# Kernel optimization log

Measured on AMD Instinct MI355X. Metric: run time of the kernel, lower is better.

Reference implementation:

```python
import jax, jax.numpy as jnp
import numpy as np

HASH_CODE_LEN = 8  # config['hash_code_len']
EPS = 1e-12

def _l2norm(x):
    n = jnp.sqrt(jnp.sum(x * x, axis=-1, keepdims=True))
    return x / jnp.maximum(n, EPS)

def setup_inputs() -> dict:
    key = jax.random.key(0)
    k1, k2, k3, k4 = jax.random.split(key, 4)
    B, H, S, D = 2, 12, 2048, 64
    Q = jax.random.normal(k1, (B, H, S, D), dtype=jnp.float32)
    K = jax.random.normal(k2, (B, H, S, D), dtype=jnp.float32)
    V = jax.random.normal(k3, (B, H, S, D), dtype=jnp.float32)
    mask = jnp.ones((B, S), dtype=jnp.float32)
    conv_w = jax.random.normal(k4, (H, 1, 3, 1), dtype=jnp.float32)  # depthwise Conv2d weight [H,1,w,1]
    return {"Q": Q, "K": K, "V": V, "mask": mask, "conv_w": conv_w}

def reference(Q, K, V, mask, conv_w):
    B, H, S, D = Q.shape
    # conv branch: depthwise conv over the sequence axis, per head (groups=num_head)
    Vm = V * mask[:, None, :, None]  # [B,H,S,D]
    conv_V = jax.lax.conv_general_dilated(
        Vm, conv_w,
        window_strides=(1, 1),
        padding=[(1, 1), (0, 0)],  # (conv_window//2, 0)
        dimension_numbers=("NCHW", "OIHW", "NCHW"),
        feature_group_count=H,
    )
    # YOSO attention: exact expectation of LSH cumulation.
    # collision prob of unit vectors q,k over hash_code_len bits: (1 - acos(q.k)/pi)^tau
    qn = _l2norm(Q)
    kn = _l2norm(K)
    dots = jnp.einsum("bhsd,bhtd->bhst", qn, kn)
    dots = jnp.clip(dots, -1.0, 1.0)
    W = (1.0 - jnp.arccos(dots) / jnp.pi) ** HASH_CODE_LEN  # [B,H,S,S]
    W = W * mask[:, None, None, :]  # key mask
    X = jnp.einsum("bhst,bhtd->bhsd", W, V)
    X = X * mask[:, None, :, None]  # query mask
    X = _l2norm(X)  # kernel.normalize(X)
    return X + conv_V
```

## Files before the change

### kernel.cpp

```cpp
#include <hip/hip_runtime.h>
#include <hip/hip_bf16.h>
#include <math.h>

#define NB 2
#define NH 12
#define NS 2048
#define ND 64
#define NBH (NB * NH)
#define TILE_USHORT 4096
#define QK_TILE_BLOCKS 1536
#define V_BLOCKS (NBH * 32)

typedef __attribute__((ext_vector_type(8))) short short8;
typedef __attribute__((ext_vector_type(4))) float floatx4;
typedef __attribute__((ext_vector_type(2))) float float2v;

__device__ __forceinline__ unsigned short f32_to_bf16_rne(float f) {
  unsigned int u = __float_as_uint(f);
  u += 0x7fffu + ((u >> 16) & 1u);
  return (unsigned short)(u >> 16);
}

__device__ __forceinline__ unsigned int bf16rne_bits(float f) {
  unsigned int u = __float_as_uint(f);
  return u + 0x7fffu + ((u >> 16) & 1u);
}

__device__ __forceinline__ unsigned int pack2_bf16_rne(float lo, float hi) {
  return __builtin_amdgcn_perm(bf16rne_bits(hi), bf16rne_bits(lo), 0x07060302);
}

__device__ __forceinline__ unsigned int pack_bf16_trunc(float lo, float hi) {
  return __builtin_amdgcn_perm(__float_as_uint(hi), __float_as_uint(lo), 0x07060302);
}

__device__ __forceinline__ float2v mk2(float x) { return (float2v){x, x}; }
__device__ __forceinline__ float2v max2(float2v a, float2v b) {
  return (float2v){fmaxf(a[0], b[0]), fmaxf(a[1], b[1])};
}
__device__ __forceinline__ float2v abs2(float2v a) {
  return (float2v){fabsf(a[0]), fabsf(a[1])};
}

__device__ __forceinline__ float yoso_f_exact(float d) {
  const float c0 = 0.49996030f;
  const float c1 = -0.06751822f;
  const float c2 = 0.02363774f;
  const float c3 = -0.00596174f;
  float a = fminf(fabsf(d), 1.0f);
  float p = fmaf(fmaf(fmaf(c3, a, c2), a, c1), a, c0);
  float u = sqrtf(1.0f - a) * p;
  return (d >= 0.0f) ? (1.0f - u) : u;
}

__device__ __forceinline__ void gload_lds16(const unsigned short* src,
                                            unsigned short* lds_dst) {
  __builtin_amdgcn_global_load_lds(
      (const __attribute__((address_space(1))) unsigned int*)(const void*)src,
      (__attribute__((address_space(3))) unsigned int*)(void*)lds_dst,
      16, 0, 0);
}

__global__ __launch_bounds__(256) void prep_all(
    const float* __restrict__ Q, const float* __restrict__ K,
    const float* __restrict__ V, const float* __restrict__ mask,
    unsigned short* __restrict__ qimg, unsigned short* __restrict__ kimg,
    unsigned short* __restrict__ vimg) {
  int blk = blockIdx.x;
  if (blk < QK_TILE_BLOCKS) {
    const float* src = Q;
    unsigned short* dst = qimg;
    if (blk >= 768) { src = K; dst = kimg; blk -= 768; }
    int ti  = blk;
    int tid = threadIdx.x;
    int w   = tid >> 6;
    int l   = tid & 63;
    int nl  = l & 15;
    int dq  = l >> 4;

    const float* row = src + ((size_t)ti * 64 + w * 16 + nl) * ND + dq * 8;
    float4 a0 = *(const float4*)(row);
    float4 a1 = *(const float4*)(row + 4);
    float4 b0 = *(const float4*)(row + 32);
    float4 b1 = *(const float4*)(row + 36);

    float ss = a0.x*a0.x + a0.y*a0.y + a0.z*a0.z + a0.w*a0.w
             + a1.x*a1.x + a1.y*a1.y + a1.z*a1.z + a1.w*a1.w
             + b0.x*b0.x + b0.y*b0.y + b0.z*b0.z + b0.w*b0.w
             + b1.x*b1.x + b1.y*b1.y + b1.z*b1.z + b1.w*b1.w;
    ss += __shfl_xor(ss, 16, 64);
    ss += __shfl_xor(ss, 32, 64);
    float rn = 1.0f / fmaxf(sqrtf(ss), 1e-12f);

    uint4 o0, o1;
    o0.x = pack2_bf16_rne(a0.x * rn, a0.y * rn);
    o0.y = pack2_bf16_rne(a0.z * rn, a0.w * rn);
    o0.z = pack2_bf16_rne(a1.x * rn, a1.y * rn);
    o0.w = pack2_bf16_rne(a1.z * rn, a1.w * rn);
    o1.x = pack2_bf16_rne(b0.x * rn, b0.y * rn);
    o1.y = pack2_bf16_rne(b0.z * rn, b0.w * rn);
    o1.z = pack2_bf16_rne(b1.x * rn, b1.y * rn);
    o1.w = pack2_bf16_rne(b1.z * rn, b1.w * rn);

    unsigned short* op = dst + (size_t)ti * TILE_USHORT + w * 512 + l * 8;
    *(uint4*)(op)            = o0;
    *(uint4*)(op + 4 * 512)  = o1;
  } else {
    int vb = blk - QK_TILE_BLOCKS;
    int bh = vb >> 5, kt = vb & 31, t0 = kt * 64;
    int b  = bh / NH;
    __shared__ float sT[64][65];
    int tid = threadIdx.x;
    int tr = tid >> 2;
    int dc = (tid & 3) * 16;
    float m = mask[b * NS + t0 + tr];
    const float* vp = V + ((size_t)bh * NS + t0 + tr) * ND + dc;
    #pragma unroll
    for (int jj = 0; jj < 16; jj += 4) {
      float4 v = *(const float4*)(vp + jj);
      sT[dc + jj + 0][tr] = v.x * m;
      sT[dc + jj + 1][tr] = v.y * m;
      sT[dc + jj + 2][tr] = v.z * m;
      sT[dc + jj + 3][tr] = v.w * m;
    }
    __syncthreads();
    int dr = tid >> 2;
    unsigned short* op = vimg + (size_t)(bh * 32 + kt) * TILE_USHORT;
    #pragma unroll
    for (int g = 0; g < 2; ++g) {
      int combo = (tid & 3) * 2 + g;
      int kk2 = combo >> 2;
      int qd  = combo & 3;
      uint4 u;
      int tb = kk2 * 32 + qd * 4;
      u.x = (unsigned int)f32_to_bf16_rne(sT[dr][tb + 0]) |
            ((unsigned int)f32_to_bf16_rne(sT[dr][tb + 1]) << 16);
      u.y = (unsigned int)f32_to_bf16_rne(sT[dr][tb + 2]) |
            ((unsigned int)f32_to_bf16_rne(sT[dr][tb + 3]) << 16);
      u.z = (unsigned int)f32_to_bf16_rne(sT[dr][tb + 16]) |
            ((unsigned int)f32_to_bf16_rne(sT[dr][tb + 17]) << 16);
      u.w = (unsigned int)f32_to_bf16_rne(sT[dr][tb + 18]) |
            ((unsigned int)f32_to_bf16_rne(sT[dr][tb + 19]) << 16);
      int frag = kk2 * 4 + (dr >> 4);
      int ln   = qd * 16 + (dr & 15);
      *(uint4*)(op + frag * 512 + ln * 8) = u;
    }
  }
}

__global__ __launch_bounds__(512, 6) void yoso_main(
    const unsigned short* __restrict__ qimg, const unsigned short* __restrict__ kimg,
    const unsigned short* __restrict__ vimg, const float* __restrict__ V,
    const float* __restrict__ mask, const float* __restrict__ conv_w,
    float* __restrict__ out) {
  int bid = blockIdx.x;
  int lid = (bid & 7) * 96 + (bid >> 3);
  int bh = lid >> 5;
  int b  = bh / NH;
  int h  = bh % NH;
  int qt = lid & 31;
  int s0 = qt * 64;

  __shared__ unsigned short kstage[2][4096];

  int tid  = threadIdx.x;
  int wv   = tid >> 6;
  int lane = tid & 63;
  int lq   = lane & 15;
  int quad = lane >> 4;
  int j    = wv & 3;
  int tk   = wv >> 2;

  uint4 qfrag[2];
  {
    const unsigned short* qtile = qimg + (size_t)(bh * 32 + qt) * TILE_USHORT;
    #pragma unroll
    for (int kk = 0; kk < 2; ++kk)
      qfrag[kk] = *(const uint4*)(qtile + (kk * 4 + j) * 512 + lane * 8);
  }

  float w0 = conv_w[h * 3 + 0], w1 = conv_w[h * 3 + 1], w2 = conv_w[h * 3 + 2];

  floatx4 acc[4];
  #pragma unroll
  for (int fd = 0; fd < 4; ++fd) acc[fd] = (floatx4){0.f, 0.f, 0.f, 0.f};

  const unsigned short* kb  = kimg + (size_t)bh * 32 * TILE_USHORT;
  const unsigned short* vbI = vimg + (size_t)bh * 32 * TILE_USHORT;

  const float P0 = 0.3183098862f;
  const float P1 = 0.0530516477f;
  const float P2 = 0.0238732415f;
  const float P3 = 0.0142098402f;
  const float P4 = 0.0096701727f;
  const float P5 = 0.0071212906f;

  auto stage_tile = [&](int buf, int kt) {
    gload_lds16(kb + (size_t)kt * TILE_USHORT + wv * 512 + lane * 8,
                &kstage[buf][wv * 512]);
  };

  stage_tile(0, 0);
  __syncthreads();

  #pragma unroll 1
  for (int kt = 0; kt < 32; ++kt) {
    int cur = kt & 1;
    if (kt < 31) stage_tile(cur ^ 1, kt + 1);

    const unsigned short* sb = kstage[cur];

    uint4 kf[2][2];
    #pragma unroll
    for (int kk = 0; kk < 2; ++kk)
      #pragma unroll
      for (int fl = 0; fl < 2; ++fl)
        kf[kk][fl] = *(const uint4*)(sb + (kk * 4 + tk * 2 + fl) * 512 + lane * 8);

    floatx4 sc[2];
    #pragma unroll
    for (int fl = 0; fl < 2; ++fl) sc[fl] = (floatx4){0.f, 0.f, 0.f, 0.f};
    #pragma unroll
    for (int kk = 0; kk < 2; ++kk) {
      short8 bq = *(const short8*)&qfrag[kk];
      #pragma unroll
      for (int fl = 0; fl < 2; ++fl)
        sc[fl] = __builtin_amdgcn_mfma_f32_16x16x32_bf16(
            *(const short8*)&kf[kk][fl], bq, sc[fl], 0, 0, 0);
    }

    const unsigned short* vtile = vbI + (size_t)kt * TILE_USHORT;
    uint4 vf[4];
    #pragma unroll
    for (int fd = 0; fd < 4; ++fd)
      vf[fd] = *(const uint4*)(vtile + (tk * 4 + fd) * 512 + lane * 8);

    {
      float2v mxy = mk2(0.f);
      #pragma unroll
      for (int fl = 0; fl < 2; ++fl) {
        float2v* p = (float2v*)&sc[fl];
        mxy = max2(mxy, max2(abs2(p[0]), abs2(p[1])));
      }
      float mx = fmaxf(mxy[0], mxy[1]);
      if (__builtin_expect(__any(mx > 0.82f), 0)) {
        #pragma unroll
        for (int fl = 0; fl < 2; ++fl)
          #pragma unroll
          for (int r2 = 0; r2 < 4; ++r2) {
            float f = yoso_f_exact(sc[fl][r2]);
            float f2 = f * f;
            float f4 = f2 * f2;
            sc[fl][r2] = f4 * f4;
          }
      } else {
        float2v c5 = mk2(P5), c4 = mk2(P4), c3 = mk2(P3), c2 = mk2(P2),
                c1 = mk2(P1), c0 = mk2(P0), hf = mk2(0.5f);
        #pragma unroll
        for (int fl = 0; fl < 2; ++fl) {
          float2v* p = (float2v*)&sc[fl];
          #pragma unroll
          for (int hh = 0; hh < 2; ++hh) {
            float2v d = p[hh];
            float2v y = d * d;
            float2v pp = ((((c5 * y + c4) * y + c3) * y + c2) * y + c1) * y + c0;
            float2v f = pp * d + hf;
            float2v f2 = f * f;
            float2v f4 = f2 * f2;
            p[hh] = f4 * f4;
          }
        }
      }
    }

    {
      uint4 u;
      u.x = pack_bf16_trunc(sc[0][0], sc[0][1]);
      u.y = pack_bf16_trunc(sc[0][2], sc[0][3]);
      u.z = pack_bf16_trunc(sc[1][0], sc[1][1]);
      u.w = pack_bf16_trunc(sc[1][2], sc[1][3]);
      short8 bw = *(short8*)&u;
      #pragma unroll
      for (int fd = 0; fd < 4; ++fd)
        acc[fd] = __builtin_amdgcn_mfma_f32_16x16x32_bf16(
            *(const short8*)&vf[fd], bw, acc[fd], 0, 0, 0);
    }

    __syncthreads();
  }

  float* xch = (float*)&kstage[0][0];
  if (tk == 1) {
    float* wr = xch + (j << 10);
    #pragma unroll
    for (int fd = 0; fd < 4; ++fd)
      #pragma unroll
      for (int r2 = 0; r2 < 4; ++r2)
        wr[(fd * 16 + quad * 4 + r2) * 16 + lq] = acc[fd][r2];
  }
  __syncthreads();
  if (tk == 0) {
    const float* rd = xch + (j << 10);
    #pragma unroll
    for (int fd = 0; fd < 4; ++fd)
      #pragma unroll
      for (int r2 = 0; r2 < 4; ++r2)
        acc[fd][r2] += rd[(fd * 16 + quad * 4 + r2) * 16 + lq];

    int s = s0 + j * 16 + lq;
    float qm  = mask[b * NS + s];
    float qm0 = (s > 0) ? mask[b * NS + s - 1] : 0.f;
    float qm2 = (s < NS - 1) ? mask[b * NS + s + 1] : 0.f;
    float ssum = 0.f;
    #pragma unroll
    for (int fd = 0; fd < 4; ++fd)
      #pragma unroll
      for (int r2 = 0; r2 < 4; ++r2) {
        float x = acc[fd][r2] * qm;
        acc[fd][r2] = x;
        ssum += x * x;
      }
    ssum += __shfl_xor(ssum, 16, 64);
    ssum += __shfl_xor(ssum, 32, 64);
    float rn = 1.0f / fmaxf(sqrtf(ssum), 1e-12f);

    const float* vfull = V + ((size_t)bh * NS + s) * ND;
    #pragma unroll
    for (int fd = 0; fd < 4; ++fd) {
      int d = fd * 16 + quad * 4;
      float4 vc1 = *(const float4*)(vfull + d);
      float4 cv;
      cv.x = w1 * vc1.x * qm; cv.y = w1 * vc1.y * qm;
      cv.z = w1 * vc1.z * qm; cv.w = w1 * vc1.w * qm;
      if (s > 0) {
        float4 vc0 = *(const float4*)(vfull - ND + d);
        cv.x += w0 * vc0.x * qm0; cv.y += w0 * vc0.y * qm0;
        cv.z += w0 * vc0.z * qm0; cv.w += w0 * vc0.w * qm0;
      }
      if (s < NS - 1) {
        float4 vc2 = *(const float4*)(vfull + ND + d);
        cv.x += w2 * vc2.x * qm2; cv.y += w2 * vc2.y * qm2;
        cv.z += w2 * vc2.z * qm2; cv.w += w2 * vc2.w * qm2;
      }
      float4 o;
      o.x = acc[fd][0] * rn + cv.x;
      o.y = acc[fd][1] * rn + cv.y;
      o.z = acc[fd][2] * rn + cv.z;
      o.w = acc[fd][3] * rn + cv.w;
      *(float4*)(out + ((size_t)bh * NS + s) * ND + d) = o;
    }
  }
}

extern "C" void kernel_launch(void* const* d_in, const int* in_sizes, int n_in,
                              void* d_out, int out_size, void* d_ws, size_t ws_size,
                              hipStream_t stream) {
  const float* Q      = (const float*)d_in[0];
  const float* K      = (const float*)d_in[1];
  const float* V      = (const float*)d_in[2];
  const float* mask   = (const float*)d_in[3];
  const float* conv_w = (const float*)d_in[4];
  float* out = (float*)d_out;

  const size_t seg = (size_t)NBH * NS * ND * sizeof(unsigned short);
  unsigned short* qimg = (unsigned short*)d_ws;
  unsigned short* kimg = (unsigned short*)((char*)d_ws + seg);
  unsigned short* vimg = (unsigned short*)((char*)d_ws + 2 * seg);

  prep_all<<<QK_TILE_BLOCKS + V_BLOCKS, 256, 0, stream>>>(Q, K, V, mask, qimg, kimg, vimg);
  yoso_main<<<NBH * 32, 512, 0, stream>>>(qimg, kimg, vimg, V, mask, conv_w, out);
}
```

Before: 136.7 us.

## Replace LDS-staged K tiles with register double-buffered direct global loads

Drops the per-block LDS staging of K tiles via global_load_lds and the per-iteration __syncthreads. Each wave now loads its K and V fragments straight from global into registers, ping-ponging between two register sets and unrolling the loop by two. The goal is to remove barrier stalls and LDS round trips. The cost is more registers, so the occupancy hint is lowered from 6 to 4, and every wave now fetches K from global memory on its own.

```diff
diff --git a/kernel.cpp b/kernel.cpp
--- a/kernel.cpp
+++ b/kernel.cpp
@@ -51,14 +51,6 @@
   float p = fmaf(fmaf(fmaf(c3, a, c2), a, c1), a, c0);
   float u = sqrtf(1.0f - a) * p;
   return (d >= 0.0f) ? (1.0f - u) : u;
-}
-
-__device__ __forceinline__ void gload_lds16(const unsigned short* src,
-                                            unsigned short* lds_dst) {
-  __builtin_amdgcn_global_load_lds(
-      (const __attribute__((address_space(1))) unsigned int*)(const void*)src,
-      (__attribute__((address_space(3))) unsigned int*)(void*)lds_dst,
-      16, 0, 0);
 }
 
 __global__ __launch_bounds__(256) void prep_all(
@@ -148,7 +140,7 @@
   }
 }
 
-__global__ __launch_bounds__(512, 6) void yoso_main(
+__global__ __launch_bounds__(512, 4) void yoso_main(
     const unsigned short* __restrict__ qimg, const unsigned short* __restrict__ kimg,
     const unsigned short* __restrict__ vimg, const float* __restrict__ V,
     const float* __restrict__ mask, const float* __restrict__ conv_w,
@@ -161,7 +153,7 @@
   int qt = lid & 31;
   int s0 = qt * 64;
 
-  __shared__ unsigned short kstage[2][4096];
+  __shared__ float xch[4][1024];
 
   int tid  = threadIdx.x;
   int wv   = tid >> 6;
@@ -195,28 +187,22 @@
   const float P4 = 0.0096701727f;
   const float P5 = 0.0071212906f;
 
-  auto stage_tile = [&](int buf, int kt) {
-    gload_lds16(kb + (size_t)kt * TILE_USHORT + wv * 512 + lane * 8,
-                &kstage[buf][wv * 512]);
+  auto load_k = [&](uint4 kf[2][2], int kt) {
+    const unsigned short* kt_ = kb + (size_t)kt * TILE_USHORT;
+    #pragma unroll
+    for (int kk = 0; kk < 2; ++kk)
+      #pragma unroll
+      for (int fl = 0; fl < 2; ++fl)
+        kf[kk][fl] = *(const uint4*)(kt_ + (kk * 4 + tk * 2 + fl) * 512 + lane * 8);
   };
-
-  stage_tile(0, 0);
-  __syncthreads();
-
-  #pragma unroll 1
-  for (int kt = 0; kt < 32; ++kt) {
-    int cur = kt & 1;
-    if (kt < 31) stage_tile(cur ^ 1, kt + 1);
-
-    const unsigned short* sb = kstage[cur];
-
-    uint4 kf[2][2];
-    #pragma unroll
-    for (int kk = 0; kk < 2; ++kk)
-      #pragma unroll
-      for (int fl = 0; fl < 2; ++fl)
-        kf[kk][fl] = *(const uint4*)(sb + (kk * 4 + tk * 2 + fl) * 512 + lane * 8);
-
+  auto load_v = [&](uint4 vf[4], int kt) {
+    const unsigned short* vt_ = vbI + (size_t)kt * TILE_USHORT;
+    #pragma unroll
+    for (int fd = 0; fd < 4; ++fd)
+      vf[fd] = *(const uint4*)(vt_ + (tk * 4 + fd) * 512 + lane * 8);
+  };
+
+  auto tile_compute = [&](const uint4 kf[2][2], const uint4 vf[4]) {
     floatx4 sc[2];
     #pragma unroll
     for (int fl = 0; fl < 2; ++fl) sc[fl] = (floatx4){0.f, 0.f, 0.f, 0.f};
@@ -228,12 +214,6 @@
         sc[fl] = __builtin_amdgcn_mfma_f32_16x16x32_bf16(
             *(const short8*)&kf[kk][fl], bq, sc[fl], 0, 0, 0);
     }
-
-    const unsigned short* vtile = vbI + (size_t)kt * TILE_USHORT;
-    uint4 vf[4];
-    #pragma unroll
-    for (int fd = 0; fd < 4; ++fd)
-      vf[fd] = *(const uint4*)(vtile + (tk * 4 + fd) * 512 + lane * 8);
 
     {
       float2v mxy = mk2(0.f);
@@ -273,25 +253,32 @@
       }
     }
 
-    {
-      uint4 u;
-      u.x = pack_bf16_trunc(sc[0][0], sc[0][1]);
-      u.y = pack_bf16_trunc(sc[0][2], sc[0][3]);
-      u.z = pack_bf16_trunc(sc[1][0], sc[1][1]);
-      u.w = pack_bf16_trunc(sc[1][2], sc[1][3]);
-      short8 bw = *(short8*)&u;
-      #pragma unroll
-      for (int fd = 0; fd < 4; ++fd)
-        acc[fd] = __builtin_amdgcn_mfma_f32_16x16x32_bf16(
-            *(const short8*)&vf[fd], bw, acc[fd], 0, 0, 0);
-    }
-
-    __syncthreads();
-  }
-
-  float* xch = (float*)&kstage[0][0];
+    uint4 u;
+    u.x = pack_bf16_trunc(sc[0][0], sc[0][1]);
+    u.y = pack_bf16_trunc(sc[0][2], sc[0][3]);
+    u.z = pack_bf16_trunc(sc[1][0], sc[1][1]);
+    u.w = pack_bf16_trunc(sc[1][2], sc[1][3]);
+    short8 bw = *(short8*)&u;
+    #pragma unroll
+    for (int fd = 0; fd < 4; ++fd)
+      acc[fd] = __builtin_amdgcn_mfma_f32_16x16x32_bf16(
+          *(const short8*)&vf[fd], bw, acc[fd], 0, 0, 0);
+  };
+
+  uint4 kfA[2][2], kfB[2][2], vfA[4], vfB[4];
+  load_k(kfA, 0);
+  #pragma unroll 1
+  for (int kt = 0; kt < 32; kt += 2) {
+    load_v(vfA, kt);
+    load_k(kfB, kt + 1);
+    tile_compute(kfA, vfA);
+    load_v(vfB, kt + 1);
+    if (kt < 30) load_k(kfA, kt + 2);
+    tile_compute(kfB, vfB);
+  }
+
   if (tk == 1) {
-    float* wr = xch + (j << 10);
+    float* wr = &xch[j][0];
     #pragma unroll
     for (int fd = 0; fd < 4; ++fd)
       #pragma unroll
@@ -300,7 +287,7 @@
   }
   __syncthreads();
   if (tk == 0) {
-    const float* rd = xch + (j << 10);
+    const float* rd = &xch[j][0];
     #pragma unroll
     for (int fd = 0; fd < 4; ++fd)
       #pragma unroll
```

Measured after the change: 142.3 us. +4.1%, slower.

## Deepen K staging to four buffers and prefetch K fragments one tile ahead

Applied to the files above, without the earlier changes.

Raises the K tile LDS ring from 2 to 4 buffers and unrolls the key loop by two. K fragments for the next tile are read from LDS into registers, and the next tile's staging is issued, before the current tile is computed. Launch bounds drop from 6 to 4 blocks per SM, allowing more registers for the doubled fragment buffers. The aim is to hide global-to-LDS and LDS-to-register latency behind the MFMA work, at the cost of lower occupancy and twice the shared memory.

```diff
diff --git a/kernel.cpp b/kernel.cpp
--- a/kernel.cpp
+++ b/kernel.cpp
@@ -148,7 +148,7 @@
   }
 }
 
-__global__ __launch_bounds__(512, 6) void yoso_main(
+__global__ __launch_bounds__(512, 4) void yoso_main(
     const unsigned short* __restrict__ qimg, const unsigned short* __restrict__ kimg,
     const unsigned short* __restrict__ vimg, const float* __restrict__ V,
     const float* __restrict__ mask, const float* __restrict__ conv_w,
@@ -161,7 +161,7 @@
   int qt = lid & 31;
   int s0 = qt * 64;
 
-  __shared__ unsigned short kstage[2][4096];
+  __shared__ unsigned short kstage[4][4096];
 
   int tid  = threadIdx.x;
   int wv   = tid >> 6;
@@ -199,24 +199,21 @@
     gload_lds16(kb + (size_t)kt * TILE_USHORT + wv * 512 + lane * 8,
                 &kstage[buf][wv * 512]);
   };
-
-  stage_tile(0, 0);
-  __syncthreads();
-
-  #pragma unroll 1
-  for (int kt = 0; kt < 32; ++kt) {
-    int cur = kt & 1;
-    if (kt < 31) stage_tile(cur ^ 1, kt + 1);
-
-    const unsigned short* sb = kstage[cur];
-
-    uint4 kf[2][2];
+  auto load_kf = [&](uint4 kf[2][2], int buf) {
+    const unsigned short* sb = kstage[buf];
     #pragma unroll
     for (int kk = 0; kk < 2; ++kk)
       #pragma unroll
       for (int fl = 0; fl < 2; ++fl)
         kf[kk][fl] = *(const uint4*)(sb + (kk * 4 + tk * 2 + fl) * 512 + lane * 8);
-
+  };
+  auto load_v = [&](uint4 vf[4], int kt) {
+    const unsigned short* vt_ = vbI + (size_t)kt * TILE_USHORT;
+    #pragma unroll
+    for (int fd = 0; fd < 4; ++fd)
+      vf[fd] = *(const uint4*)(vt_ + (tk * 4 + fd) * 512 + lane * 8);
+  };
+  auto tile_compute = [&](const uint4 kf[2][2], const uint4 vf[4]) {
     floatx4 sc[2];
     #pragma unroll
     for (int fl = 0; fl < 2; ++fl) sc[fl] = (floatx4){0.f, 0.f, 0.f, 0.f};
@@ -228,12 +225,6 @@
         sc[fl] = __builtin_amdgcn_mfma_f32_16x16x32_bf16(
             *(const short8*)&kf[kk][fl], bq, sc[fl], 0, 0, 0);
     }
-
-    const unsigned short* vtile = vbI + (size_t)kt * TILE_USHORT;
-    uint4 vf[4];
-    #pragma unroll
-    for (int fd = 0; fd < 4; ++fd)
-      vf[fd] = *(const uint4*)(vtile + (tk * 4 + fd) * 512 + lane * 8);
 
     {
       float2v mxy = mk2(0.f);
@@ -273,19 +264,37 @@
       }
     }
 
-    {
-      uint4 u;
-      u.x = pack_bf16_trunc(sc[0][0], sc[0][1]);
-      u.y = pack_bf16_trunc(sc[0][2], sc[0][3]);
-      u.z = pack_bf16_trunc(sc[1][0], sc[1][1]);
-      u.w = pack_bf16_trunc(sc[1][2], sc[1][3]);
-      short8 bw = *(short8*)&u;
-      #pragma unroll
-      for (int fd = 0; fd < 4; ++fd)
-        acc[fd] = __builtin_amdgcn_mfma_f32_16x16x32_bf16(
-            *(const short8*)&vf[fd], bw, acc[fd], 0, 0, 0);
-    }
-
+    uint4 u;
+    u.x = pack_bf16_trunc(sc[0][0], sc[0][1]);
+    u.y = pack_bf16_trunc(sc[0][2], sc[0][3]);
+    u.z = pack_bf16_trunc(sc[1][0], sc[1][1]);
+    u.w = pack_bf16_trunc(sc[1][2], sc[1][3]);
+    short8 bw = *(short8*)&u;
+    #pragma unroll
+    for (int fd = 0; fd < 4; ++fd)
+      acc[fd] = __builtin_amdgcn_mfma_f32_16x16x32_bf16(
+          *(const short8*)&vf[fd], bw, acc[fd], 0, 0, 0);
+  };
+
+  stage_tile(0, 0);
+  stage_tile(1, 1);
+  __syncthreads();
+
+  uint4 kfA[2][2], kfB[2][2], vfA[4], vfB[4];
+  load_kf(kfA, 0);
+
+  #pragma unroll 1
+  for (int kt = 0; kt < 32; kt += 2) {
+    load_v(vfA, kt);
+    if (kt + 2 < 32) stage_tile((kt + 2) & 3, kt + 2);
+    load_kf(kfB, (kt + 1) & 3);
+    tile_compute(kfA, vfA);
+    __syncthreads();
+
+    load_v(vfB, kt + 1);
+    if (kt + 3 < 32) stage_tile((kt + 3) & 3, kt + 3);
+    if (kt + 2 < 32) load_kf(kfA, (kt + 2) & 3);
+    tile_compute(kfB, vfB);
     __syncthreads();
   }
 
```

Result: slower. 149.3 us (+9.2%).
